# Performance work log

Measured on AMD Instinct MI355X. Metric: run time of the kernel, lower is better.

## Reference

```python
import jax, jax.numpy as jnp
import numpy as np

B, N, D_IN, D_OUT = 4096, 200, 64, 64


def setup_inputs() -> dict:
    key = jax.random.key(0)
    k1, k2 = jax.random.split(key)
    x = jax.random.normal(k1, (B, N, D_IN), dtype=jnp.float32)
    # weight initialized like TF add_weight default (glorot-ish scale via normal here)
    weight = jax.random.normal(k2, (1, N, D_IN, D_OUT), dtype=jnp.float32) * (1.0 / np.sqrt(D_IN))
    bias = jnp.zeros((1, N, D_OUT), dtype=jnp.float32)
    return {"x": x, "weight": weight, "bias": bias}


def reference(x, weight, bias):
    # Original: (x[..., None] * weight).sum(-2) + bias
    # == per-token matmul: out[b,n,o] = sum_i x[b,n,i] * weight[0,n,i,o] + bias[0,n,o]
    out = jnp.einsum('bni,nio->bno', x, weight[0])
    return out + bias
```

## Files before the change

### kernel.cpp

```cpp
#include <hip/hip_runtime.h>


#define B_DIM 4096
#define N_DIM 200
#define D 64
#define ROWS_PER_BLOCK 128
#define CHUNK 32
#define NWAVES 4
#define ROWS_PER_WAVE (CHUNK / NWAVES)

__global__ __launch_bounds__(256, 4)
void nlinear_kernel(const float* __restrict__ x,
                    const float* __restrict__ w,
                    const float* __restrict__ bias,
                    float* __restrict__ out) {
    const int n    = blockIdx.y;
    const int b0   = blockIdx.x * ROWS_PER_BLOCK;
    const int tid  = threadIdx.x;
    const int lane = tid & 63;
    const int wave = tid >> 6;

    __shared__ float x_lds[CHUNK][D];

    const float* wn = w + (size_t)n * (D * D);
    float wreg[D];
#pragma unroll
    for (int i = 0; i < D; ++i) wreg[i] = wn[i * D + lane];

    const float bv = bias[n * D + lane];

    const size_t row_stride = (size_t)N_DIM * D;
    const float* xb = x   + (size_t)b0 * row_stride + (size_t)n * D;
    float*       ob = out + (size_t)b0 * row_stride + (size_t)n * D;

    for (int c0 = 0; c0 < ROWS_PER_BLOCK; c0 += CHUNK) {
#pragma unroll
        for (int k = 0; k < 2; ++k) {
            const int idx = tid + k * 256;
            const int r   = idx >> 4;
            const int f   = (idx & 15) << 2;
            const float4 v = *(const float4*)(xb + (size_t)(c0 + r) * row_stride + f);
            *(float4*)(&x_lds[r][f]) = v;
        }
        __syncthreads();

#pragma unroll
        for (int rr = 0; rr < ROWS_PER_WAVE; ++rr) {
            const int r = wave * ROWS_PER_WAVE + rr;
            const float* xr = &x_lds[r][0];
            float a0 = 0.f, a1 = 0.f, a2 = 0.f, a3 = 0.f;
#pragma unroll
            for (int i = 0; i < D; i += 16) {
                const float4 v0 = *(const float4*)(xr + i);
                const float4 v1 = *(const float4*)(xr + i + 4);
                const float4 v2 = *(const float4*)(xr + i + 8);
                const float4 v3 = *(const float4*)(xr + i + 12);
                a0 = fmaf(v0.x, wreg[i + 0], a0);
                a0 = fmaf(v0.y, wreg[i + 1], a0);
                a0 = fmaf(v0.z, wreg[i + 2], a0);
                a0 = fmaf(v0.w, wreg[i + 3], a0);
                a1 = fmaf(v1.x, wreg[i + 4], a1);
                a1 = fmaf(v1.y, wreg[i + 5], a1);
                a1 = fmaf(v1.z, wreg[i + 6], a1);
                a1 = fmaf(v1.w, wreg[i + 7], a1);
                a2 = fmaf(v2.x, wreg[i + 8], a2);
                a2 = fmaf(v2.y, wreg[i + 9], a2);
                a2 = fmaf(v2.z, wreg[i + 10], a2);
                a2 = fmaf(v2.w, wreg[i + 11], a2);
                a3 = fmaf(v3.x, wreg[i + 12], a3);
                a3 = fmaf(v3.y, wreg[i + 13], a3);
                a3 = fmaf(v3.z, wreg[i + 14], a3);
                a3 = fmaf(v3.w, wreg[i + 15], a3);
            }
            ob[(size_t)(c0 + r) * row_stride + lane] = ((a0 + a1) + (a2 + a3)) + bv;
        }
        __syncthreads();
    }
}

extern "C" void kernel_launch(void* const* d_in, const int* in_sizes, int n_in,
                              void* d_out, int out_size, void* d_ws, size_t ws_size,
                              hipStream_t stream) {
    const float* x    = (const float*)d_in[0];
    const float* w    = (const float*)d_in[1];
    const float* bias = (const float*)d_in[2];
    float*       out  = (float*)d_out;

    dim3 grid(B_DIM / ROWS_PER_BLOCK, N_DIM);
    nlinear_kernel<<<grid, dim3(256), 0, stream>>>(x, w, bias, out);
}
```

Before: 440.7 us.

## Use split-bf16 MFMA (3-pass) for per-token matmul instead of scalar FMA

```diff
diff --git a/kernel.cpp b/kernel.cpp
--- a/kernel.cpp
+++ b/kernel.cpp
@@ -4,88 +4,125 @@
 #define B_DIM 4096
 #define N_DIM 200
 #define D 64
-#define ROWS_PER_BLOCK 128
-#define CHUNK 32
-#define NWAVES 4
-#define ROWS_PER_WAVE (CHUNK / NWAVES)
 
-__global__ __launch_bounds__(256, 4)
-void nlinear_kernel(const float* __restrict__ x,
-                    const float* __restrict__ w,
-                    const float* __restrict__ bias,
-                    float* __restrict__ out) {
-    const int n    = blockIdx.y;
-    const int b0   = blockIdx.x * ROWS_PER_BLOCK;
-    const int tid  = threadIdx.x;
-    const int lane = tid & 63;
-    const int wave = tid >> 6;
+typedef __attribute__((ext_vector_type(8))) short bf16x8;
+typedef __attribute__((ext_vector_type(4))) float f32x4;
 
-    __shared__ float x_lds[CHUNK][D];
+__device__ __forceinline__ unsigned bf16_rne(float f) {
+  unsigned u = __float_as_uint(f);
+  return (u + 0x7fffu + ((u >> 16) & 1u)) >> 16;
+}
 
-    const float* wn = w + (size_t)n * (D * D);
-    float wreg[D];
+__device__ __forceinline__ void cvt_split8(const float4 a, const float4 b,
+                                           bf16x8& h, bf16x8& l) {
+  float f[8] = {a.x, a.y, a.z, a.w, b.x, b.y, b.z, b.w};
 #pragma unroll
-    for (int i = 0; i < D; ++i) wreg[i] = wn[i * D + lane];
+  for (int j = 0; j < 8; ++j) {
+    const unsigned hb = bf16_rne(f[j]);
+    const float r = f[j] - __uint_as_float(hb << 16);
+    const unsigned lb = bf16_rne(r);
+    h[j] = (short)hb;
+    l[j] = (short)lb;
+  }
+}
 
-    const float bv = bias[n * D + lane];
+__global__ __launch_bounds__(256, 2)
+void nlinear_mfma(const float* __restrict__ x,
+                  const float* __restrict__ w,
+                  const float* __restrict__ bias,
+                  float* __restrict__ out) {
+  const int n    = blockIdx.y;
+  const int tid  = threadIdx.x;
+  const int lane = tid & 63;
+  const int wave = tid >> 6;
+  const int c    = lane & 15;
+  const int kg   = lane >> 4;
 
-    const size_t row_stride = (size_t)N_DIM * D;
-    const float* xb = x   + (size_t)b0 * row_stride + (size_t)n * D;
-    float*       ob = out + (size_t)b0 * row_stride + (size_t)n * D;
+  __shared__ float w_lds[D * D];
+  __shared__ float b_lds[D];
 
-    for (int c0 = 0; c0 < ROWS_PER_BLOCK; c0 += CHUNK) {
+  {
+    const float4* src = (const float4*)(w + (size_t)n * (D * D));
+    float4* dst = (float4*)w_lds;
 #pragma unroll
-        for (int k = 0; k < 2; ++k) {
-            const int idx = tid + k * 256;
-            const int r   = idx >> 4;
-            const int f   = (idx & 15) << 2;
-            const float4 v = *(const float4*)(xb + (size_t)(c0 + r) * row_stride + f);
-            *(float4*)(&x_lds[r][f]) = v;
-        }
-        __syncthreads();
+    for (int k = 0; k < 4; ++k) dst[tid + 256 * k] = src[tid + 256 * k];
+    if (tid < 16)
+      ((float4*)b_lds)[tid] = ((const float4*)(bias + (size_t)n * D))[tid];
+  }
+  __syncthreads();
+
+  bf16x8 Wh[2][4], Wl[2][4];
+#pragma unroll
+  for (int ks = 0; ks < 2; ++ks) {
+#pragma unroll
+    for (int nf = 0; nf < 4; ++nf) {
+#pragma unroll
+      for (int j = 0; j < 8; ++j) {
+        const int i = ks * 32 + kg * 8 + j;
+        const float v = w_lds[i * D + nf * 16 + c];
+        const unsigned hb = bf16_rne(v);
+        const float r = v - __uint_as_float(hb << 16);
+        const unsigned lb = bf16_rne(r);
+        Wh[ks][nf][j] = (short)hb;
+        Wl[ks][nf][j] = (short)lb;
+      }
+    }
+  }
+
+  const size_t rstride = (size_t)N_DIM * D;
+  const int row0 = blockIdx.x * 256 + wave * 64;
+  const float* xb = x + (size_t)row0 * rstride + (size_t)n * D;
+  float* ob = out + (size_t)row0 * rstride + (size_t)n * D;
+
+  const float bv[4] = {b_lds[c], b_lds[16 + c], b_lds[32 + c], b_lds[48 + c]};
 
 #pragma unroll
-        for (int rr = 0; rr < ROWS_PER_WAVE; ++rr) {
-            const int r = wave * ROWS_PER_WAVE + rr;
-            const float* xr = &x_lds[r][0];
-            float a0 = 0.f, a1 = 0.f, a2 = 0.f, a3 = 0.f;
+  for (int mf = 0; mf < 4; ++mf) {
+    const float* xr = xb + (size_t)(mf * 16 + c) * rstride + kg * 8;
+    const float4 v0 = *(const float4*)(xr);
+    const float4 v1 = *(const float4*)(xr + 4);
+    const float4 v2 = *(const float4*)(xr + 32);
+    const float4 v3 = *(const float4*)(xr + 36);
+    bf16x8 ah[2], al[2];
+    cvt_split8(v0, v1, ah[0], al[0]);
+    cvt_split8(v2, v3, ah[1], al[1]);
+
+    f32x4 acc[4];
 #pragma unroll
-            for (int i = 0; i < D; i += 16) {
-                const float4 v0 = *(const float4*)(xr + i);
-                const float4 v1 = *(const float4*)(xr + i + 4);
-                const float4 v2 = *(const float4*)(xr + i + 8);
-                const float4 v3 = *(const float4*)(xr + i + 12);
-                a0 = fmaf(v0.x, wreg[i + 0], a0);
-                a0 = fmaf(v0.y, wreg[i + 1], a0);
-                a0 = fmaf(v0.z, wreg[i + 2], a0);
-                a0 = fmaf(v0.w, wreg[i + 3], a0);
-                a1 = fmaf(v1.x, wreg[i + 4], a1);
-                a1 = fmaf(v1.y, wreg[i + 5], a1);
-                a1 = fmaf(v1.z, wreg[i + 6], a1);
-                a1 = fmaf(v1.w, wreg[i + 7], a1);
-                a2 = fmaf(v2.x, wreg[i + 8], a2);
-                a2 = fmaf(v2.y, wreg[i + 9], a2);
-                a2 = fmaf(v2.z, wreg[i + 10], a2);
-                a2 = fmaf(v2.w, wreg[i + 11], a2);
-                a3 = fmaf(v3.x, wreg[i + 12], a3);
-                a3 = fmaf(v3.y, wreg[i + 13], a3);
-                a3 = fmaf(v3.z, wreg[i + 14], a3);
-                a3 = fmaf(v3.w, wreg[i + 15], a3);
-            }
-            ob[(size_t)(c0 + r) * row_stride + lane] = ((a0 + a1) + (a2 + a3)) + bv;
-        }
-        __syncthreads();
+    for (int nf = 0; nf < 4; ++nf) {
+      f32x4 t = {bv[nf], bv[nf], bv[nf], bv[nf]};
+      acc[nf] = t;
     }
+
+#pragma unroll
+    for (int ks = 0; ks < 2; ++ks) {
+#pragma unroll
+      for (int nf = 0; nf < 4; ++nf) {
+        acc[nf] = __builtin_amdgcn_mfma_f32_16x16x32_bf16(ah[ks], Wh[ks][nf], acc[nf], 0, 0, 0);
+        acc[nf] = __builtin_amdgcn_mfma_f32_16x16x32_bf16(ah[ks], Wl[ks][nf], acc[nf], 0, 0, 0);
+        acc[nf] = __builtin_amdgcn_mfma_f32_16x16x32_bf16(al[ks], Wh[ks][nf], acc[nf], 0, 0, 0);
+      }
+    }
+
+    float* orow = ob + (size_t)(mf * 16 + kg * 4) * rstride;
+#pragma unroll
+    for (int nf = 0; nf < 4; ++nf) {
+#pragma unroll
+      for (int j = 0; j < 4; ++j) {
+        orow[(size_t)j * rstride + nf * 16 + c] = acc[nf][j];
+      }
+    }
+  }
 }
 
 extern "C" void kernel_launch(void* const* d_in, const int* in_sizes, int n_in,
                               void* d_out, int out_size, void* d_ws, size_t ws_size,
                               hipStream_t stream) {
-    const float* x    = (const float*)d_in[0];
-    const float* w    = (const float*)d_in[1];
-    const float* bias = (const float*)d_in[2];
-    float*       out  = (float*)d_out;
+  const float* x    = (const float*)d_in[0];
+  const float* w    = (const float*)d_in[1];
+  const float* bias = (const float*)d_in[2];
+  float*       out  = (float*)d_out;
 
-    dim3 grid(B_DIM / ROWS_PER_BLOCK, N_DIM);
-    nlinear_kernel<<<grid, dim3(256), 0, stream>>>(x, w, bias, out);
+  dim3 grid(B_DIM / 256, N_DIM);
+  nlinear_mfma<<<grid, dim3(256), 0, stream>>>(x, w, bias, out);
 }
```

New measurement: 373.5 us. 1.18x faster.
